# Kernel optimization log

Hardware: AMD Instinct MI355X
Metric: run time of the kernel (lower is better)

Reference implementation:

```python
import jax, jax.numpy as jnp
import numpy as np
import itertools

CONVEX_K = 10
NUM_CLASS = 100
B, N = 8, 16384
MINDIS_INIT = 1.0e5  # torch code initializes mindis to 100000


def _hull_vertex_labels_np(pts):
    """pts: [G, K, 3] numpy. Exact brute-force 3D convex hull vertex labels
    (general position): a triple is a hull facet iff all points lie on one
    side of its plane; every point on some facet is a hull vertex."""
    G, K, _ = pts.shape
    tri = np.array(list(itertools.combinations(range(K), 3)))  # [T,3]
    a = pts[:, tri[:, 0]]                                      # [G,T,3]
    b = pts[:, tri[:, 1]]
    c = pts[:, tri[:, 2]]
    n = np.cross(b - a, c - a)                                 # [G,T,3]
    d = np.einsum('gkd,gtd->gtk', pts, n) - np.einsum('gtd,gtd->gt', a, n)[:, :, None]
    eps = 1e-7
    facet = (d <= eps).all(-1) | (d >= -eps).all(-1)           # [G,T]
    labels = np.zeros((G, K), dtype=np.int32)
    gidx, tidx = np.nonzero(facet)
    for col in range(3):
        labels[gidx, tri[tidx, col]] = 1
    return labels


def setup_inputs() -> dict:
    key = jax.random.key(0)
    k1, k2, k3 = jax.random.split(key, 3)
    xyz = jax.random.normal(k1, (B, N, 6), dtype=jnp.float32)
    skel_xyz = jax.random.normal(k2, (B, NUM_CLASS * CONVEX_K, 3), dtype=jnp.float32)
    weights = jax.random.normal(k3, (B, NUM_CLASS * CONVEX_K // CONVEX_K * CONVEX_K,), dtype=jnp.float32)[:, :NUM_CLASS * CONVEX_K].reshape(B, -1)[:, :1000]
    weights = jax.random.normal(k3, (B, NUM_CLASS * CONVEX_K), dtype=jnp.float32)
    skel_np = np.asarray(skel_xyz).reshape(B * NUM_CLASS, CONVEX_K, 3)
    labels = jnp.asarray(_hull_vertex_labels_np(skel_np).reshape(B, NUM_CLASS, CONVEX_K))
    return {"xyz": xyz, "skel_xyz": skel_xyz, "weights": weights,
            "labels": labels, "num_class": NUM_CLASS}


def reference(xyz, skel_xyz, weights, labels, num_class):
    b = xyz.shape[0]
    pts = xyz[:, :, :3]                                   # [B,N,3]; normals xyz[:,:,3:6] unused
    cp = skel_xyz.reshape(b, num_class, CONVEX_K, 3)      # [B,C,K,3]

    # --- convex loss: for each non-vertex point, min sq-dist to a hull vertex ---
    diff = cp[:, :, :, None, :] - cp[:, :, None, :, :]    # [B,C,K,K,3] (small)
    sqd = jnp.sum(diff * diff, axis=-1)                   # [B,C,K,K]
    is_vert = labels == 1                                  # [B,C,K]
    masked = jnp.where(is_vert[:, :, None, :], sqd, jnp.inf)
    mindis = jnp.minimum(jnp.min(masked, axis=-1), MINDIS_INIT)  # [B,C,K]
    loss_convex = jnp.sum(jnp.where(is_vert, 0.0, mindis)) / (b * num_class)

    # --- Chamfer (closest_distance_with_batch both directions, L2 norm, summed) ---
    skel = skel_xyz                                        # [B,M,3]
    d2 = (jnp.sum(pts * pts, -1)[:, :, None]
          + jnp.sum(skel * skel, -1)[:, None, :]
          - 2.0 * jnp.einsum('bnd,bmd->bnm', pts, skel))   # [B,N,M]
    d = jnp.sqrt(jnp.maximum(d2, 1e-12))
    loss_cd = (jnp.sum(jnp.min(d, axis=2)) + jnp.sum(jnp.min(d, axis=1))) / b

    return 1.0 * loss_convex + 0.1 * loss_cd
```

## Files before the change

kernel.cpp:

```cpp
#include <hip/hip_runtime.h>

#define BATCH 8
#define NPTS 16384
#define MSKEL 1000
#define NCLS 100
#define CKK 10
#define MINDIS_INITF 100000.0f

#define OFF_PTSM 32000
#define OFF_MINB (32000 + 524288)

__global__ __launch_bounds__(256) void k_prep(const float* __restrict__ xyz,
                                              const float* __restrict__ skel,
                                              float4* __restrict__ skelN,
                                              float4* __restrict__ ptsM,
                                              unsigned int* __restrict__ minbits,
                                              float* __restrict__ out) {
    const int gid = blockIdx.x * 256 + threadIdx.x;
    {
        const float* p = xyz + (size_t)gid * 6;
        float x = p[0], y = p[1], z = p[2];
        ptsM[gid] = make_float4(x, y, z, 0.5f * (x * x + y * y + z * z));
    }
    if (gid < BATCH * MSKEL) {
        const float* s = skel + (size_t)gid * 3;
        float sx = s[0], sy = s[1], sz = s[2];
        skelN[gid] = make_float4(-sx, -sy, -sz, 0.5f * (sx * sx + sy * sy + sz * sz));
        minbits[gid] = 0x7F800000u;
    }
    if (gid == 0) out[0] = 0.0f;
}

__global__ __launch_bounds__(256) void k_chamfer(const float4* __restrict__ skelN,
                                                 const float4* __restrict__ ptsM,
                                                 unsigned int* __restrict__ minbits,
                                                 float* __restrict__ out) {
    const int bid = blockIdx.x;
    const int tid = threadIdx.x;
    const int wave = tid >> 6, lane = tid & 63;

    if (bid < 256) {
        const int b = bid >> 5, tile = bid & 31;
        const float4* __restrict__ base = ptsM + b * NPTS + tile * 512;

        float4 P[8];
        float mt[8];
#pragma unroll
        for (int j = 0; j < 8; ++j) {
            P[j] = base[j * 64 + lane];
            mt[j] = 3.4e38f;
        }

        const float4* __restrict__ sk = skelN + b * MSKEL + wave * 250;
#pragma unroll 5
        for (int m = 0; m < 250; ++m) {
            float4 s = sk[m];
#pragma unroll
            for (int j = 0; j < 8; ++j) {
                float t = fmaf(P[j].x, s.x, fmaf(P[j].y, s.y, fmaf(P[j].z, s.z, s.w)));
                mt[j] = fminf(mt[j], t);
            }
        }

        __shared__ float sm[4 * 512];
#pragma unroll
        for (int j = 0; j < 8; ++j) {
            sm[wave * 512 + j * 64 + lane] = mt[j] + P[j].w;
        }
        __syncthreads();

        float a0 = fminf(fminf(sm[tid], sm[512 + tid]),
                         fminf(sm[1024 + tid], sm[1536 + tid]));
        float a1 = fminf(fminf(sm[tid + 256], sm[512 + tid + 256]),
                         fminf(sm[1024 + tid + 256], sm[1536 + tid + 256]));
        float d = sqrtf(fmaxf(2.0f * a0, 1e-12f)) + sqrtf(fmaxf(2.0f * a1, 1e-12f));

#pragma unroll
        for (int o = 32; o > 0; o >>= 1) d += __shfl_down(d, o, 64);
        __shared__ float s_part[4];
        if (lane == 0) s_part[wave] = d;
        __syncthreads();
        if (tid == 0) {
            atomicAdd(out, 0.0125f * (s_part[0] + s_part[1] + s_part[2] + s_part[3]));
        }
    } else {
        const int id = bid - 256;
        const int b = id >> 5, tile = id & 31;
        const int cover = tid >> 7;
        const int local = tid & 127;
        const int m0 = local * 8;

        float4 S[8];
        float mind[8];
#pragma unroll
        for (int k = 0; k < 8; ++k) {
            const int m = m0 + k;
            S[k] = (m < MSKEL) ? skelN[b * MSKEL + m]
                               : make_float4(0.0f, 0.0f, 0.0f, 0.0f);
            mind[k] = 3.4e38f;
        }

        const float4* __restrict__ pp = ptsM + b * NPTS + tile * 512 + cover * 256;
#pragma unroll 4
        for (int n = 0; n < 256; ++n) {
            float4 r = pp[n];
#pragma unroll
            for (int k = 0; k < 8; ++k) {
                float t = fmaf(r.x, S[k].x, fmaf(r.y, S[k].y, fmaf(r.z, S[k].z, r.w)));
                mind[k] = fminf(mind[k], t);
            }
        }
#pragma unroll
        for (int k = 0; k < 8; ++k) {
            const int m = m0 + k;
            if (m < MSKEL) {
                float d2 = 2.0f * (mind[k] + S[k].w);
                atomicMin(&minbits[b * MSKEL + m], __float_as_uint(fmaxf(d2, 0.0f)));
            }
        }
    }
}

__global__ __launch_bounds__(256) void k_reduce(const float* __restrict__ skel,
                                                const int* __restrict__ labels,
                                                const unsigned int* __restrict__ minbits,
                                                float* __restrict__ out) {
    const int gid = blockIdx.x * 256 + threadIdx.x;
    const int tid = threadIdx.x;
    float acc = 0.0f;

    for (int i = gid; i < BATCH * MSKEL; i += 2048) {
        acc += 0.0125f * sqrtf(fmaxf(__uint_as_float(minbits[i]), 1e-12f));
    }

    if (gid < BATCH * NCLS) {
        const int b = gid / NCLS, c = gid - b * NCLS;
        const float* cp = skel + ((size_t)b * MSKEL + c * CKK) * 3;
        const int* lab = labels + (size_t)b * NCLS * CKK + c * CKK;
        float x[CKK], y[CKK], z[CKK];
        int lv[CKK];
#pragma unroll
        for (int i = 0; i < CKK; ++i) {
            x[i] = cp[i * 3 + 0]; y[i] = cp[i * 3 + 1]; z[i] = cp[i * 3 + 2];
            lv[i] = lab[i];
        }
        float convexSum = 0.0f;
#pragma unroll
        for (int i = 0; i < CKK; ++i) {
            if (lv[i] != 1) {
                float mind = MINDIS_INITF;
#pragma unroll
                for (int j = 0; j < CKK; ++j) {
                    if (lv[j] == 1) {
                        float dx = x[i] - x[j], dy = y[i] - y[j], dz = z[i] - z[j];
                        mind = fminf(mind, dx * dx + dy * dy + dz * dz);
                    }
                }
                convexSum += mind;
            }
        }
        acc += convexSum * (1.0f / (BATCH * NCLS));
    }

#pragma unroll
    for (int o = 32; o > 0; o >>= 1) acc += __shfl_down(acc, o, 64);
    __shared__ float s_part[4];
    const int wave = tid >> 6, lane = tid & 63;
    if (lane == 0) s_part[wave] = acc;
    __syncthreads();
    if (tid == 0) {
        atomicAdd(out, s_part[0] + s_part[1] + s_part[2] + s_part[3]);
    }
}

extern "C" void kernel_launch(void* const* d_in, const int* in_sizes, int n_in,
                              void* d_out, int out_size, void* d_ws, size_t ws_size,
                              hipStream_t stream) {
    const float* xyz = (const float*)d_in[0];
    const float* skel = (const float*)d_in[1];
    const int* labels = (const int*)d_in[3];
    float* out = (float*)d_out;

    float4* skelN = (float4*)d_ws;
    float4* ptsM = (float4*)((float*)d_ws + OFF_PTSM);
    unsigned int* minbits = (unsigned int*)((float*)d_ws + OFF_MINB);

    k_prep<<<512, 256, 0, stream>>>(xyz, skel, skelN, ptsM, minbits, out);
    k_chamfer<<<512, 256, 0, stream>>>(skelN, ptsM, minbits, out);
    k_reduce<<<8, 256, 0, stream>>>(skel, labels, minbits, out);
}
```

Baseline: 112.5 us.

## Split chamfer work into more blocks and replace atomics with partial-min buffers

Doubles the chamfer grid to 1024 blocks. Each point block now scans half of the skeleton set, and each skeleton block handles 4 skeleton points over a 256-point tile. The float atomicMin and atomicAdd reductions are replaced by per-half and per-tile partial minimum arrays written to workspace. A wider reduce kernel then combines these with the sqrt and sum. The aim is better occupancy and load balance on the GPU and no atomic contention, at the cost of extra global writes and a heavier final reduction pass.

```diff
diff --git a/kernel.cpp b/kernel.cpp
--- a/kernel.cpp
+++ b/kernel.cpp
@@ -8,13 +8,13 @@
 #define MINDIS_INITF 100000.0f
 
 #define OFF_PTSM 32000
-#define OFF_MINB (32000 + 524288)
+#define OFF_NMIN (32000 + 524288)
+#define OFF_MTIL (32000 + 524288 + 262144)
 
 __global__ __launch_bounds__(256) void k_prep(const float* __restrict__ xyz,
                                               const float* __restrict__ skel,
                                               float4* __restrict__ skelN,
                                               float4* __restrict__ ptsM,
-                                              unsigned int* __restrict__ minbits,
                                               float* __restrict__ out) {
     const int gid = blockIdx.x * 256 + threadIdx.x;
     {
@@ -26,21 +26,23 @@
         const float* s = skel + (size_t)gid * 3;
         float sx = s[0], sy = s[1], sz = s[2];
         skelN[gid] = make_float4(-sx, -sy, -sz, 0.5f * (sx * sx + sy * sy + sz * sz));
-        minbits[gid] = 0x7F800000u;
     }
     if (gid == 0) out[0] = 0.0f;
 }
 
 __global__ __launch_bounds__(256) void k_chamfer(const float4* __restrict__ skelN,
                                                  const float4* __restrict__ ptsM,
-                                                 unsigned int* __restrict__ minbits,
-                                                 float* __restrict__ out) {
+                                                 float* __restrict__ nMins,
+                                                 float* __restrict__ mTile) {
     const int bid = blockIdx.x;
     const int tid = threadIdx.x;
     const int wave = tid >> 6, lane = tid & 63;
 
-    if (bid < 256) {
-        const int b = bid >> 5, tile = bid & 31;
+    if (bid < 512) {
+        const int b = bid >> 6;
+        const int sub = bid & 63;
+        const int tile = sub >> 1;
+        const int half = sub & 1;
         const float4* __restrict__ base = ptsM + b * NPTS + tile * 512;
 
         float4 P[8];
@@ -51,9 +53,9 @@
             mt[j] = 3.4e38f;
         }
 
-        const float4* __restrict__ sk = skelN + b * MSKEL + wave * 250;
+        const float4* __restrict__ sk = skelN + b * MSKEL + half * 500 + wave * 125;
 #pragma unroll 5
-        for (int m = 0; m < 250; ++m) {
+        for (int m = 0; m < 125; ++m) {
             float4 s = sk[m];
 #pragma unroll
             for (int j = 0; j < 8; ++j) {
@@ -73,64 +75,68 @@
                          fminf(sm[1024 + tid], sm[1536 + tid]));
         float a1 = fminf(fminf(sm[tid + 256], sm[512 + tid + 256]),
                          fminf(sm[1024 + tid + 256], sm[1536 + tid + 256]));
-        float d = sqrtf(fmaxf(2.0f * a0, 1e-12f)) + sqrtf(fmaxf(2.0f * a1, 1e-12f));
+        float* dst = nMins + half * (BATCH * NPTS) + b * NPTS + tile * 512;
+        dst[tid] = a0;
+        dst[tid + 256] = a1;
+    } else {
+        const int id = bid - 512;
+        const int b = id >> 6, tile = id & 63;
+        const int m0 = tid * 4;
 
+        float4 S[4];
+        float mind[4];
 #pragma unroll
-        for (int o = 32; o > 0; o >>= 1) d += __shfl_down(d, o, 64);
-        __shared__ float s_part[4];
-        if (lane == 0) s_part[wave] = d;
-        __syncthreads();
-        if (tid == 0) {
-            atomicAdd(out, 0.0125f * (s_part[0] + s_part[1] + s_part[2] + s_part[3]));
-        }
-    } else {
-        const int id = bid - 256;
-        const int b = id >> 5, tile = id & 31;
-        const int cover = tid >> 7;
-        const int local = tid & 127;
-        const int m0 = local * 8;
-
-        float4 S[8];
-        float mind[8];
-#pragma unroll
-        for (int k = 0; k < 8; ++k) {
+        for (int k = 0; k < 4; ++k) {
             const int m = m0 + k;
-            S[k] = (m < MSKEL) ? skelN[b * MSKEL + m]
-                               : make_float4(0.0f, 0.0f, 0.0f, 0.0f);
+            const int mi = (m < MSKEL) ? m : (MSKEL - 1);
+            S[k] = skelN[b * MSKEL + mi];
             mind[k] = 3.4e38f;
         }
 
-        const float4* __restrict__ pp = ptsM + b * NPTS + tile * 512 + cover * 256;
-#pragma unroll 4
+        const float4* __restrict__ pp = ptsM + b * NPTS + tile * 256;
+#pragma unroll 8
         for (int n = 0; n < 256; ++n) {
             float4 r = pp[n];
 #pragma unroll
-            for (int k = 0; k < 8; ++k) {
+            for (int k = 0; k < 4; ++k) {
                 float t = fmaf(r.x, S[k].x, fmaf(r.y, S[k].y, fmaf(r.z, S[k].z, r.w)));
                 mind[k] = fminf(mind[k], t);
             }
         }
-#pragma unroll
-        for (int k = 0; k < 8; ++k) {
-            const int m = m0 + k;
-            if (m < MSKEL) {
-                float d2 = 2.0f * (mind[k] + S[k].w);
-                atomicMin(&minbits[b * MSKEL + m], __float_as_uint(fmaxf(d2, 0.0f)));
-            }
-        }
+        float4 v = make_float4(mind[0] + S[0].w, mind[1] + S[1].w,
+                               mind[2] + S[2].w, mind[3] + S[3].w);
+        float4* dst = (float4*)(mTile + (size_t)(b * 64 + tile) * 1024);
+        dst[tid] = v;
     }
 }
 
 __global__ __launch_bounds__(256) void k_reduce(const float* __restrict__ skel,
                                                 const int* __restrict__ labels,
-                                                const unsigned int* __restrict__ minbits,
+                                                const float* __restrict__ nMins,
+                                                const float* __restrict__ mTile,
                                                 float* __restrict__ out) {
     const int gid = blockIdx.x * 256 + threadIdx.x;
     const int tid = threadIdx.x;
     float acc = 0.0f;
 
-    for (int i = gid; i < BATCH * MSKEL; i += 2048) {
-        acc += 0.0125f * sqrtf(fmaxf(__uint_as_float(minbits[i]), 1e-12f));
+#pragma unroll
+    for (int it = 0; it < 8; ++it) {
+        const int i = gid + it * 16384;
+        float a = fminf(nMins[i], nMins[BATCH * NPTS + i]);
+        acc += 0.0125f * sqrtf(fmaxf(2.0f * a, 1e-12f));
+    }
+
+    if (gid < BATCH * 1024) {
+        const int b = gid >> 10, m = gid & 1023;
+        if (m < MSKEL) {
+            const float* src = mTile + (size_t)b * 64 * 1024 + m;
+            float mn = 3.4e38f;
+#pragma unroll 8
+            for (int t = 0; t < 64; ++t) {
+                mn = fminf(mn, src[t * 1024]);
+            }
+            acc += 0.0125f * sqrtf(fmaxf(2.0f * mn, 1e-12f));
+        }
     }
 
     if (gid < BATCH * NCLS) {
@@ -183,9 +189,10 @@
 
     float4* skelN = (float4*)d_ws;
     float4* ptsM = (float4*)((float*)d_ws + OFF_PTSM);
-    unsigned int* minbits = (unsigned int*)((float*)d_ws + OFF_MINB);
+    float* nMins = (float*)d_ws + OFF_NMIN;
+    float* mTile = (float*)d_ws + OFF_MTIL;
 
-    k_prep<<<512, 256, 0, stream>>>(xyz, skel, skelN, ptsM, minbits, out);
-    k_chamfer<<<512, 256, 0, stream>>>(skelN, ptsM, minbits, out);
-    k_reduce<<<8, 256, 0, stream>>>(skel, labels, minbits, out);
+    k_prep<<<512, 256, 0, stream>>>(xyz, skel, skelN, ptsM, out);
+    k_chamfer<<<1024, 256, 0, stream>>>(skelN, ptsM, nMins, mTile);
+    k_reduce<<<64, 256, 0, stream>>>(skel, labels, nMins, mTile, out);
 }
```

New measurement: 106.2 us. 1.06x faster.
